# Performance work log

Hardware: AMD Instinct MI355X
Metric: run time of the kernel (lower is better)

## Reference

```python
import jax, jax.numpy as jnp
import numpy as np

D = 3            # sde dimension
M_I = 20         # gaussians per axis -> m = M_I**D = 8000
K = 16384        # batch of positions
SIGMA_I = 1.0    # scalar covariance diagonal
NORMALIZED = True


def _grid_means():
    # uniform grid over domain [-3, 3]^D, matching np.mgrid with m_i points per axis
    axes = [np.linspace(-3.0, 3.0, M_I) for _ in range(D)]
    g = np.stack(np.meshgrid(*axes, indexing='ij'), axis=-1).reshape(-1, D)
    return jnp.asarray(g, dtype=jnp.float32)


def setup_inputs() -> dict:
    key = jax.random.key(0)
    kx, kt = jax.random.split(key)
    x = jax.random.normal(kx, (K, D), dtype=jnp.float32)
    means = _grid_means()                      # (m, d)
    theta = jax.random.normal(kt, (means.shape[0],), dtype=jnp.float32)
    return {"x": x, "means": means, "theta": theta}


def reference(x, means, theta):
    # x: (K, d), means: (m, d), theta: (m,)
    sigma = jnp.float32(SIGMA_I)
    diff = x[:, None, :] - means[None, :, :]                  # (K, m, d)
    log_basis = -0.5 * jnp.sum(diff * diff, axis=2) / sigma   # (K, m)
    if NORMALIZED:
        log_basis = log_basis - jnp.float32(np.log(2.0 * np.pi * SIGMA_I) * D / 2.0)
    basis = jnp.exp(log_basis)                                # (K, m)
    # grad basis = -(diff / sigma) * basis[..., None]; weighted sum over m
    out = -jnp.einsum('kmd,km,m->kd', diff, basis, theta) / sigma
    return out
```

## Files before the change

kernel.cpp:

```cpp
#include <hip/hip_runtime.h>


#define NG   20
#define MTOT 8000
#define KPB  256
#define IC   2
#define NCHUNK (NG / IC)

__global__ __launch_bounds__(KPB) void gauss_factored_kernel(
    const float* __restrict__ x, const float* __restrict__ means,
    const float* __restrict__ theta, float* __restrict__ out) {
  __shared__ float sth[MTOT];
  __shared__ float sg[3 * NG];

  const int tid = threadIdx.x;

  {
    const float4* th4 = (const float4*)theta;
    float4* sth4 = (float4*)sth;
    for (int idx = tid; idx < MTOT / 4; idx += KPB) sth4[idx] = th4[idx];
  }
  if (tid < 3 * NG) {
    int axis = tid / NG, p = tid % NG;
    int m = (axis == 0) ? p * 400 : (axis == 1) ? p * 20 : p;
    sg[tid] = means[m * 3 + axis];
  }
  __syncthreads();

  const int k = blockIdx.x * KPB + tid;
  const float x0 = x[k * 3 + 0];
  const float x1 = x[k * 3 + 1];
  const float x2 = x[k * 3 + 2];

  float Ey[NG], Eyp[NG], Ez[NG], Ezp[NG];
#pragma unroll
  for (int j = 0; j < NG; ++j) {
    float dy = x1 - sg[NG + j];
    float e = __expf(-0.5f * dy * dy);
    Ey[j] = e;
    Eyp[j] = -dy * e;
  }
#pragma unroll
  for (int l = 0; l < NG; ++l) {
    float dz = x2 - sg[2 * NG + l];
    float e = __expf(-0.5f * dz * dz);
    Ez[l] = e;
    Ezp[l] = -dz * e;
  }

  float o0 = 0.f, o1 = 0.f, o2 = 0.f;
  const int i0 = blockIdx.y * IC;

#pragma unroll
  for (int ii = 0; ii < IC; ++ii) {
    const int i = i0 + ii;
    const float dxv = x0 - sg[i];
    const float ex = __expf(-0.5f * dxv * dxv);
    const float exn = -dxv * ex;

    float b = 0.f, b1 = 0.f, b2 = 0.f;
    const float* thrown = &sth[i * 400];
#pragma unroll
    for (int j = 0; j < NG; ++j) {
      const float4* trow = (const float4*)(thrown + j * NG);
      float aZ0 = 0.f, aZ1 = 0.f, aZp0 = 0.f, aZp1 = 0.f;
#pragma unroll
      for (int l4 = 0; l4 < 5; ++l4) {
        const float4 t = trow[l4];
        aZ0  = fmaf(t.x, Ez [4 * l4 + 0], aZ0);
        aZp0 = fmaf(t.x, Ezp[4 * l4 + 0], aZp0);
        aZ1  = fmaf(t.y, Ez [4 * l4 + 1], aZ1);
        aZp1 = fmaf(t.y, Ezp[4 * l4 + 1], aZp1);
        aZ0  = fmaf(t.z, Ez [4 * l4 + 2], aZ0);
        aZp0 = fmaf(t.z, Ezp[4 * l4 + 2], aZp0);
        aZ1  = fmaf(t.w, Ez [4 * l4 + 3], aZ1);
        aZp1 = fmaf(t.w, Ezp[4 * l4 + 3], aZp1);
      }
      const float aZ = aZ0 + aZ1;
      const float aZp = aZp0 + aZp1;
      b  = fmaf(Ey[j],  aZ,  b);
      b1 = fmaf(Eyp[j], aZ,  b1);
      b2 = fmaf(Ey[j],  aZp, b2);
    }
    o0 = fmaf(exn, b, o0);
    o1 = fmaf(ex, b1, o1);
    o2 = fmaf(ex, b2, o2);
  }

  const float Nc = 0.06349363593424097f;
  atomicAdd(&out[k * 3 + 0], o0 * Nc);
  atomicAdd(&out[k * 3 + 1], o1 * Nc);
  atomicAdd(&out[k * 3 + 2], o2 * Nc);
}

extern "C" void kernel_launch(void* const* d_in, const int* in_sizes, int n_in,
                              void* d_out, int out_size, void* d_ws, size_t ws_size,
                              hipStream_t stream) {
  const float* x = (const float*)d_in[0];
  const float* means = (const float*)d_in[1];
  const float* theta = (const float*)d_in[2];
  float* out = (float*)d_out;

  const int K = in_sizes[0] / 3;

  hipMemsetAsync(out, 0, (size_t)out_size * sizeof(float), stream);

  dim3 grid(K / KPB, NCHUNK);
  gauss_factored_kernel<<<grid, KPB, 0, stream>>>(x, means, theta, out);
}
```

Measured before the change: 70.06 us.

## Split work per x-grid index with small blocks and per-block theta slice in LDS

Each block now handles a single x-axis grid index with 64 threads, loading only a 400-element theta slice into shared memory rather than all 8000 values. The grid grows to 20 chunks along y, and the Ey exponentials are computed inline inside the j loop instead of being precomputed into arrays. This cuts LDS footprint and register pressure, which should raise occupancy and parallelism. The cost is twice as many atomic adds and redundant Ez/Ey exponentials per block.

```diff
diff --git a/kernel.cpp b/kernel.cpp
--- a/kernel.cpp
+++ b/kernel.cpp
@@ -2,29 +2,29 @@
 
 
 #define NG   20
-#define MTOT 8000
-#define KPB  256
-#define IC   2
-#define NCHUNK (NG / IC)
+#define KPB  64
 
-__global__ __launch_bounds__(KPB) void gauss_factored_kernel(
+__global__ __launch_bounds__(KPB, 4) void gauss_factored_kernel(
     const float* __restrict__ x, const float* __restrict__ means,
     const float* __restrict__ theta, float* __restrict__ out) {
-  __shared__ float sth[MTOT];
-  __shared__ float sg[3 * NG];
+  __shared__ float sth[NG * NG];
+  __shared__ float sgy[NG];
+  __shared__ float sgz[NG];
 
   const int tid = threadIdx.x;
+  const int i = blockIdx.y;
 
   {
-    const float4* th4 = (const float4*)theta;
+    const float4* th4 = (const float4*)theta + i * (NG * NG / 4);
     float4* sth4 = (float4*)sth;
-    for (int idx = tid; idx < MTOT / 4; idx += KPB) sth4[idx] = th4[idx];
+    for (int idx = tid; idx < NG * NG / 4; idx += KPB) sth4[idx] = th4[idx];
   }
-  if (tid < 3 * NG) {
-    int axis = tid / NG, p = tid % NG;
-    int m = (axis == 0) ? p * 400 : (axis == 1) ? p * 20 : p;
-    sg[tid] = means[m * 3 + axis];
+  if (tid < 2 * NG) {
+    const int axis = tid / NG, p = tid % NG;
+    if (axis == 0) sgy[p] = means[p * 60 + 1];
+    else           sgz[p] = means[p * 3 + 2];
   }
+  const float gi = means[i * 1200];
   __syncthreads();
 
   const int k = blockIdx.x * KPB + tid;
@@ -32,65 +32,51 @@
   const float x1 = x[k * 3 + 1];
   const float x2 = x[k * 3 + 2];
 
-  float Ey[NG], Eyp[NG], Ez[NG], Ezp[NG];
-#pragma unroll
-  for (int j = 0; j < NG; ++j) {
-    float dy = x1 - sg[NG + j];
-    float e = __expf(-0.5f * dy * dy);
-    Ey[j] = e;
-    Eyp[j] = -dy * e;
-  }
+  float Ez[NG], Ezp[NG];
 #pragma unroll
   for (int l = 0; l < NG; ++l) {
-    float dz = x2 - sg[2 * NG + l];
-    float e = __expf(-0.5f * dz * dz);
+    const float dz = x2 - sgz[l];
+    const float e = __expf(-0.5f * dz * dz);
     Ez[l] = e;
     Ezp[l] = -dz * e;
   }
 
-  float o0 = 0.f, o1 = 0.f, o2 = 0.f;
-  const int i0 = blockIdx.y * IC;
+  const float dxv = x0 - gi;
+  const float ex = __expf(-0.5f * dxv * dxv);
+  const float exn = -dxv * ex;
 
+  float b = 0.f, b1 = 0.f, b2 = 0.f;
 #pragma unroll
-  for (int ii = 0; ii < IC; ++ii) {
-    const int i = i0 + ii;
-    const float dxv = x0 - sg[i];
-    const float ex = __expf(-0.5f * dxv * dxv);
-    const float exn = -dxv * ex;
+  for (int j = 0; j < NG; ++j) {
+    const float dy = x1 - sgy[j];
+    const float ey = __expf(-0.5f * dy * dy);
 
-    float b = 0.f, b1 = 0.f, b2 = 0.f;
-    const float* thrown = &sth[i * 400];
+    const float4* trow = (const float4*)(sth + j * NG);
+    float aZ0 = 0.f, aZ1 = 0.f, aZp0 = 0.f, aZp1 = 0.f;
 #pragma unroll
-    for (int j = 0; j < NG; ++j) {
-      const float4* trow = (const float4*)(thrown + j * NG);
-      float aZ0 = 0.f, aZ1 = 0.f, aZp0 = 0.f, aZp1 = 0.f;
-#pragma unroll
-      for (int l4 = 0; l4 < 5; ++l4) {
-        const float4 t = trow[l4];
-        aZ0  = fmaf(t.x, Ez [4 * l4 + 0], aZ0);
-        aZp0 = fmaf(t.x, Ezp[4 * l4 + 0], aZp0);
-        aZ1  = fmaf(t.y, Ez [4 * l4 + 1], aZ1);
-        aZp1 = fmaf(t.y, Ezp[4 * l4 + 1], aZp1);
-        aZ0  = fmaf(t.z, Ez [4 * l4 + 2], aZ0);
-        aZp0 = fmaf(t.z, Ezp[4 * l4 + 2], aZp0);
-        aZ1  = fmaf(t.w, Ez [4 * l4 + 3], aZ1);
-        aZp1 = fmaf(t.w, Ezp[4 * l4 + 3], aZp1);
-      }
-      const float aZ = aZ0 + aZ1;
-      const float aZp = aZp0 + aZp1;
-      b  = fmaf(Ey[j],  aZ,  b);
-      b1 = fmaf(Eyp[j], aZ,  b1);
-      b2 = fmaf(Ey[j],  aZp, b2);
+    for (int l4 = 0; l4 < 5; ++l4) {
+      const float4 t = trow[l4];
+      aZ0  = fmaf(t.x, Ez [4 * l4 + 0], aZ0);
+      aZp0 = fmaf(t.x, Ezp[4 * l4 + 0], aZp0);
+      aZ1  = fmaf(t.y, Ez [4 * l4 + 1], aZ1);
+      aZp1 = fmaf(t.y, Ezp[4 * l4 + 1], aZp1);
+      aZ0  = fmaf(t.z, Ez [4 * l4 + 2], aZ0);
+      aZp0 = fmaf(t.z, Ezp[4 * l4 + 2], aZp0);
+      aZ1  = fmaf(t.w, Ez [4 * l4 + 3], aZ1);
+      aZp1 = fmaf(t.w, Ezp[4 * l4 + 3], aZp1);
     }
-    o0 = fmaf(exn, b, o0);
-    o1 = fmaf(ex, b1, o1);
-    o2 = fmaf(ex, b2, o2);
+    const float aZ = aZ0 + aZ1;
+    const float aZp = aZp0 + aZp1;
+    const float eyAZ = ey * aZ;
+    b += eyAZ;
+    b1 = fmaf(-dy, eyAZ, b1);
+    b2 = fmaf(ey, aZp, b2);
   }
 
   const float Nc = 0.06349363593424097f;
-  atomicAdd(&out[k * 3 + 0], o0 * Nc);
-  atomicAdd(&out[k * 3 + 1], o1 * Nc);
-  atomicAdd(&out[k * 3 + 2], o2 * Nc);
+  atomicAdd(&out[k * 3 + 0], exn * b * Nc);
+  atomicAdd(&out[k * 3 + 1], ex * b1 * Nc);
+  atomicAdd(&out[k * 3 + 2], ex * b2 * Nc);
 }
 
 extern "C" void kernel_launch(void* const* d_in, const int* in_sizes, int n_in,
@@ -105,6 +91,6 @@
 
   hipMemsetAsync(out, 0, (size_t)out_size * sizeof(float), stream);
 
-  dim3 grid(K / KPB, NCHUNK);
+  dim3 grid(K / KPB, NG);
   gauss_factored_kernel<<<grid, KPB, 0, stream>>>(x, means, theta, out);
 }
```

After: 74.26 us. +6.0%, slower.
